# Performance work log

Hardware: AMD Instinct MI355X
Metric: run time of the kernel (lower is better)

The kernel has to match this reference:

```python
import jax, jax.numpy as jnp
import numpy as np

D_IN, D, N_HEADS, K, VOCAB = 768, 512, 8, 6, 1000
HEAD_DIM = D // N_HEADS


def setup_inputs() -> dict:
    key = jax.random.key(0)
    ks = jax.random.split(key, 16)
    B, T, L = 32, 4096, 512
    s = 0.02
    return {
        "video_features": jax.random.normal(ks[0], (B, T, D_IN), jnp.float32),
        "input_ids": jax.random.randint(ks[1], (B, L), 0, VOCAB),
        "attention_mask": jnp.ones((B, L), jnp.float32),
        # video_encoder (Linear 768->512), stored [in, out]
        "W_enc": jax.random.normal(ks[2], (D_IN, D), jnp.float32) * s,
        "b_enc": jnp.zeros((D,), jnp.float32),
        # frame_selector (Linear 512->1)
        "W_sel": jax.random.normal(ks[3], (D, 1), jnp.float32) * s,
        "b_sel": jnp.zeros((1,), jnp.float32),
        # text_encoder embedding
        "emb": jax.random.normal(ks[4], (VOCAB, D), jnp.float32) * s,
        # MultiheadAttention in/out projections
        "W_q": jax.random.normal(ks[5], (D, D), jnp.float32) * s,
        "W_k": jax.random.normal(ks[6], (D, D), jnp.float32) * s,
        "W_v": jax.random.normal(ks[7], (D, D), jnp.float32) * s,
        "b_q": jnp.zeros((D,), jnp.float32),
        "b_k": jnp.zeros((D,), jnp.float32),
        "b_v": jnp.zeros((D,), jnp.float32),
        "W_o": jax.random.normal(ks[8], (D, D), jnp.float32) * s,
        "b_o": jnp.zeros((D,), jnp.float32),
        # classifier (Linear 512->1000)
        "W_cls": jax.random.normal(ks[9], (D, VOCAB), jnp.float32) * s,
        "b_cls": jnp.zeros((VOCAB,), jnp.float32),
    }


def reference(video_features, input_ids, attention_mask, W_enc, b_enc, W_sel,
              b_sel, emb, W_q, W_k, W_v, b_q, b_k, b_v, W_o, b_o, W_cls, b_cls):
    # encode frames: [B, T, 512]
    ve = jax.nn.relu(jnp.einsum('bti,io->bto', video_features, W_enc) + b_enc)
    # frame scores [B, T] -> top-6 gather
    scores = jnp.einsum('btd,do->bto', ve, W_sel)[..., 0] + b_sel[0]
    _, top_idx = jax.lax.top_k(scores, K)                      # [B, K]
    reps = jnp.take_along_axis(ve, top_idx[:, :, None], axis=1)  # [B, K, 512]
    # text embedding (query), reps as key/value
    txt = emb[input_ids]                                       # [B, L, 512]
    B, L, _ = txt.shape
    q = (txt @ W_q + b_q).reshape(B, L, N_HEADS, HEAD_DIM)
    k = (reps @ W_k + b_k).reshape(B, K, N_HEADS, HEAD_DIM)
    v = (reps @ W_v + b_v).reshape(B, K, N_HEADS, HEAD_DIM)
    scale = 1.0 / np.sqrt(HEAD_DIM).astype(np.float32)
    attn = jax.nn.softmax(jnp.einsum('blhd,bkhd->bhlk', q, k) * scale, axis=-1)
    ctx = jnp.einsum('bhlk,bkhd->blhd', attn, v).reshape(B, L, D)
    fused = ctx @ W_o + b_o
    logits = fused @ W_cls + b_cls                             # [B, L, 1000]
    return logits, reps
```

## Files before the change

### kernel.cpp

```cpp
#include <hip/hip_runtime.h>
#include <math.h>


#define DEV __device__ __forceinline__

typedef _Float16 half8 __attribute__((ext_vector_type(8)));
typedef float f32x4v __attribute__((ext_vector_type(4)));

DEV unsigned short f2h_bits(float f) {
  union { _Float16 h; unsigned short u; } cv;
  cv.h = (_Float16)f;
  return cv.u;
}

DEV uint4 packf16x8(float4 fa, float4 fb) {
  uint4 pk;
  pk.x = (unsigned int)f2h_bits(fa.x) | ((unsigned int)f2h_bits(fa.y) << 16);
  pk.y = (unsigned int)f2h_bits(fa.z) | ((unsigned int)f2h_bits(fa.w) << 16);
  pk.z = (unsigned int)f2h_bits(fb.x) | ((unsigned int)f2h_bits(fb.y) << 16);
  pk.w = (unsigned int)f2h_bits(fb.z) | ((unsigned int)f2h_bits(fb.w) << 16);
  return pk;
}

DEV void gload16(const void* g, void* lds) {
  auto* gp = reinterpret_cast<const __attribute__((address_space(1))) unsigned int*>(
      reinterpret_cast<unsigned long long>(g));
  auto* lp = reinterpret_cast<__attribute__((address_space(3))) unsigned int*>(
      reinterpret_cast<unsigned long long>(lds));
  __builtin_amdgcn_global_load_lds(gp, lp, 16, 0, 0);
}

__global__ __launch_bounds__(256) void prep_k(
    const float* __restrict__ W_enc, unsigned short* __restrict__ WencT,
    const float* __restrict__ emb, const float* __restrict__ W_q,
    const float* __restrict__ b_q, float* __restrict__ Qe,
    const float* __restrict__ W_o, const float* __restrict__ W_cls,
    unsigned short* __restrict__ WocT, const float* __restrict__ b_o,
    const float* __restrict__ b_cls, float* __restrict__ boc) {
  __shared__ float plds[2080];
  const int blk = blockIdx.x, tid = threadIdx.x;
  if (blk < 96) {
    unsigned short* t = (unsigned short*)plds;
    const int k0 = (blk % 12) * 64, n0 = (blk / 12) * 64;
    for (int e = tid; e < 4096; e += 256) {
      int kk = e >> 6, nn = e & 63;
      t[kk * 65 + nn] = f2h_bits(W_enc[(size_t)(k0 + kk) * 512 + n0 + nn]);
    }
    __syncthreads();
    for (int e = tid; e < 4096; e += 256) {
      int nn = e >> 6, kk = e & 63;
      WencT[(size_t)(n0 + nn) * 768 + k0 + kk] = t[kk * 65 + nn];
    }
  } else if (blk < 346) {
    float* er = plds;
    const int r0 = (blk - 96) * 4;
    for (int i = tid; i < 2048; i += 256) er[i] = emb[(size_t)r0 * 512 + i];
    __syncthreads();
    const int j0 = tid, j1 = tid + 256;
    float a0[4], a1[4];
#pragma unroll
    for (int r = 0; r < 4; ++r) { a0[r] = 0.f; a1[r] = 0.f; }
    for (int i = 0; i < 512; ++i) {
      float w0 = W_q[i * 512 + j0], w1 = W_q[i * 512 + j1];
#pragma unroll
      for (int r = 0; r < 4; ++r) {
        a0[r] += er[r * 512 + i] * w0;
        a1[r] += er[r * 512 + i] * w1;
      }
    }
    float bq0 = b_q[j0], bq1 = b_q[j1];
#pragma unroll
    for (int r = 0; r < 4; ++r) {
      Qe[(size_t)(r0 + r) * 512 + j0] = a0[r] + bq0;
      Qe[(size_t)(r0 + r) * 512 + j1] = a1[r] + bq1;
    }
  } else if (blk < 474) {
    float* wr = plds;
    const int i0 = (blk - 346) * 4;
    for (int i = tid; i < 2048; i += 256) wr[i] = W_o[(size_t)i0 * 512 + i];
    __syncthreads();
    float a[4][4];
#pragma unroll
    for (int r = 0; r < 4; ++r)
#pragma unroll
      for (int c = 0; c < 4; ++c) a[r][c] = 0.f;
    for (int m = 0; m < 512; ++m) {
      float wc[4];
#pragma unroll
      for (int c = 0; c < 4; ++c) {
        int j = tid + c * 256;
        wc[c] = (j < 1000) ? W_cls[(size_t)m * 1000 + j] : 0.f;
      }
#pragma unroll
      for (int r = 0; r < 4; ++r) {
        float x = wr[r * 512 + m];
#pragma unroll
        for (int c = 0; c < 4; ++c) a[r][c] += x * wc[c];
      }
    }
#pragma unroll
    for (int r = 0; r < 4; ++r)
#pragma unroll
      for (int c = 0; c < 4; ++c) {
        int j = tid + c * 256;
        if (j < 1000) WocT[(size_t)j * 512 + i0 + r] = f2h_bits(a[r][c]);
      }
    if (blk == 346) {
      for (int i = tid; i < 24 * 512; i += 256) WocT[512000 + i] = 0;
    }
  } else {
    int j = (blk - 474) * 256 + tid;
    float s = 0.f;
    if (j < 1000) {
      for (int m = 0; m < 512; ++m) s += b_o[m] * W_cls[(size_t)m * 1000 + j];
      s += b_cls[j];
    }
    boc[j] = s;
  }
}

__global__ __launch_bounds__(512, 2) void score_gemm(
    const float* __restrict__ vf, const unsigned short* __restrict__ WencT,
    const float* __restrict__ b_enc, const float* __restrict__ W_sel,
    const float* __restrict__ b_sel, float* __restrict__ scores) {
  __shared__ unsigned short As[2][128 * 32];
  __shared__ unsigned short Bs[2][512 * 32];
  __shared__ float red[8 * 128];

  const int tid = threadIdx.x;
  const int wv = tid >> 6, lane = tid & 63;
  const int quad = lane >> 4, l15 = lane & 15;
  const int rowBase = blockIdx.x * 128;
  const int rso = ((quad ^ (l15 & 3)) << 4);
  char* const AsB0 = (char*)As[0];
  char* const AsB1 = (char*)As[1];
  char* const BsB0 = (char*)Bs[0];
  char* const BsB1 = (char*)Bs[1];

  f32x4v acc[8][4];
#pragma unroll
  for (int i = 0; i < 8; ++i)
#pragma unroll
    for (int j = 0; j < 4; ++j) acc[i][j] = (f32x4v){0.f, 0.f, 0.f, 0.f};

  const int arow = tid >> 2, aseg = tid & 3;
  const float* aSrc = vf + (size_t)(rowBase + arow) * 768 + aseg * 8;
  const int adst = arow * 64 + ((aseg ^ (arow & 3)) << 4);

  auto stage_b = [&](int kk, char* dstB) {
#pragma unroll
    for (int it = 0; it < 4; ++it) {
      int q = tid + it * 512;
      int n = q >> 2, seg = q & 3;
      gload16(WencT + (size_t)n * 768 + kk * 32 + ((seg ^ (n & 3)) << 3),
              dstB + (it * 512 + wv * 64) * 16);
    }
  };
  auto consume = [&](const char* A, const char* B) {
    half8 af[8], bf[4];
#pragma unroll
    for (int i = 0; i < 8; ++i)
      af[i] = *(const half8*)(A + (16 * i + l15) * 64 + rso);
#pragma unroll
    for (int j = 0; j < 4; ++j)
      bf[j] = *(const half8*)(B + (wv * 64 + 16 * j + l15) * 64 + rso);
#pragma unroll
    for (int i = 0; i < 8; ++i)
#pragma unroll
      for (int j = 0; j < 4; ++j)
        acc[i][j] = __builtin_amdgcn_mfma_f32_16x16x32_f16(af[i], bf[j], acc[i][j], 0, 0, 0);
  };

  stage_b(0, BsB0);
  {
    float4 fa = *(const float4*)(aSrc);
    float4 fb = *(const float4*)(aSrc + 4);
    *(uint4*)(AsB0 + adst) = packf16x8(fa, fb);
  }
  __syncthreads();
  int cur = 0;
  for (int kk = 0; kk < 23; ++kk) {
    const float* s = aSrc + (kk + 1) * 32;
    float4 fa = *(const float4*)(s);
    float4 fb = *(const float4*)(s + 4);
    char* An = cur ? AsB0 : AsB1;
    char* Bn = cur ? BsB0 : BsB1;
    stage_b(kk + 1, Bn);
    consume(cur ? AsB1 : AsB0, cur ? BsB1 : BsB0);
    *(uint4*)(An + adst) = packf16x8(fa, fb);
    __syncthreads();
    cur ^= 1;
  }
  consume(cur ? AsB1 : AsB0, cur ? BsB1 : BsB0);

  float be[4], wsv[4];
#pragma unroll
  for (int j = 0; j < 4; ++j) {
    int col = wv * 64 + 16 * j + l15;
    be[j] = b_enc[col];
    wsv[j] = W_sel[col];
  }
  float part[32];
#pragma unroll
  for (int x = 0; x < 32; ++x) part[x] = 0.f;
#pragma unroll
  for (int i = 0; i < 8; ++i)
#pragma unroll
    for (int j = 0; j < 4; ++j)
#pragma unroll
      for (int r = 0; r < 4; ++r) {
        float v = acc[i][j][r] + be[j];
        v = fmaxf(v, 0.f);
        part[i * 4 + r] += v * wsv[j];
      }
#pragma unroll
  for (int m = 1; m < 16; m <<= 1)
#pragma unroll
    for (int x = 0; x < 32; ++x) part[x] += __shfl_xor(part[x], m);
  if (l15 == 0) {
#pragma unroll
    for (int i = 0; i < 8; ++i)
#pragma unroll
      for (int r = 0; r < 4; ++r)
        red[wv * 128 + 16 * i + quad * 4 + r] = part[i * 4 + r];
  }
  __syncthreads();
  if (tid < 128) {
    float s = 0.f;
#pragma unroll
    for (int ww = 0; ww < 8; ++ww) s += red[ww * 128 + tid];
    scores[rowBase + tid] = s + b_sel[0];
  }
}

__global__ __launch_bounds__(256) void topk16(const float* __restrict__ scores,
                                              int* __restrict__ cand) {
  __shared__ float swv[4];
  __shared__ int swi[4];
  __shared__ int winner;
  const int b = blockIdx.x, tid = threadIdx.x;
  const int lane = tid & 63, w = tid >> 6;
  float v[16];
#pragma unroll
  for (int p = 0; p < 16; ++p) v[p] = scores[b * 4096 + p * 256 + tid];
  for (int r = 0; r < 16; ++r) {
    float bv = v[0];
    int bp = 0;
#pragma unroll
    for (int p = 1; p < 16; ++p)
      if (v[p] > bv) { bv = v[p]; bp = p; }
    int bi = bp * 256 + tid;
#pragma unroll
    for (int m = 1; m < 64; m <<= 1) {
      float ov = __shfl_xor(bv, m);
      int oi = __shfl_xor(bi, m);
      if (ov > bv || (ov == bv && oi < bi)) { bv = ov; bi = oi; }
    }
    if (lane == 0) { swv[w] = bv; swi[w] = bi; }
    __syncthreads();
    if (tid == 0) {
      float fv = swv[0];
      int fi = swi[0];
#pragma unroll
      for (int x = 1; x < 4; ++x)
        if (swv[x] > fv || (swv[x] == fv && swi[x] < fi)) { fv = swv[x]; fi = swi[x]; }
      cand[b * 16 + r] = fi;
      winner = fi;
    }
    __syncthreads();
    const int wi = winner;
    const int wp = wi >> 8, wt = wi & 255;
#pragma unroll
    for (int p = 0; p < 16; ++p)
      if (p == wp && tid == wt) v[p] = -3.0e38f;
    __syncthreads();
  }
}

__global__ __launch_bounds__(256) void rescore(
    const float* __restrict__ vf, const int* __restrict__ cand,
    const float* __restrict__ W_enc, const float* __restrict__ b_enc,
    const float* __restrict__ W_sel, const float* __restrict__ b_sel,
    float* __restrict__ veC, float* __restrict__ exsc) {
  __shared__ float vfs[4][768];
  __shared__ float redl[16];
  const int b = blockIdx.x, cb = blockIdx.y * 4, tid = threadIdx.x;
  for (int c = 0; c < 4; ++c) {
    int t = cand[b * 16 + cb + c];
    const float* src = vf + ((size_t)b * 4096 + t) * 768;
    for (int i = tid; i < 768; i += 256) vfs[c][i] = src[i];
  }
  __syncthreads();
  const int j0 = tid, j1 = tid + 256;
  float a0[4] = {0.f, 0.f, 0.f, 0.f}, a1[4] = {0.f, 0.f, 0.f, 0.f};
  for (int i = 0; i < 768; ++i) {
    float w0 = W_enc[(size_t)i * 512 + j0], w1 = W_enc[(size_t)i * 512 + j1];
#pragma unroll
    for (int c = 0; c < 4; ++c) {
      float x = vfs[c][i];
      a0[c] += x * w0;
      a1[c] += x * w1;
    }
  }
  float ws0 = W_sel[j0], ws1 = W_sel[j1];
  float be0 = b_enc[j0], be1 = b_enc[j1];
  float s[4];
#pragma unroll
  for (int c = 0; c < 4; ++c) {
    float v0 = fmaxf(a0[c] + be0, 0.f);
    float v1 = fmaxf(a1[c] + be1, 0.f);
    veC[((size_t)b * 16 + cb + c) * 512 + j0] = v0;
    veC[((size_t)b * 16 + cb + c) * 512 + j1] = v1;
    s[c] = v0 * ws0 + v1 * ws1;
  }
#pragma unroll
  for (int m = 1; m < 64; m <<= 1)
#pragma unroll
    for (int c = 0; c < 4; ++c) s[c] += __shfl_xor(s[c], m);
  int w = tid >> 6;
  if ((tid & 63) == 0) {
#pragma unroll
    for (int c = 0; c < 4; ++c) redl[c * 4 + w] = s[c];
  }
  __syncthreads();
  if (tid < 4)
    exsc[b * 16 + cb + tid] = redl[tid * 4 + 0] + redl[tid * 4 + 1] +
                              redl[tid * 4 + 2] + redl[tid * 4 + 3] + b_sel[0];
}

__global__ __launch_bounds__(256) void select6(
    const float* __restrict__ exsc, const int* __restrict__ cand,
    const float* __restrict__ veC, int* __restrict__ sel,
    float* __restrict__ repsOut) {
  __shared__ int selL[6];
  const int b = blockIdx.x, tid = threadIdx.x;
  if (tid == 0) {
    float v[16]; int idx[16]; bool used[16];
    for (int c = 0; c < 16; ++c) {
      v[c] = exsc[b * 16 + c];
      idx[c] = cand[b * 16 + c];
      used[c] = false;
    }
    for (int r = 0; r < 6; ++r) {
      int bi = -1;
      for (int c = 0; c < 16; ++c) {
        if (used[c]) continue;
        if (bi < 0 || v[c] > v[bi] || (v[c] == v[bi] && idx[c] < idx[bi])) bi = c;
      }
      used[bi] = true;
      selL[r] = bi;
      sel[b * 6 + r] = bi;
    }
  }
  __syncthreads();
  for (int r = 0; r < 6; ++r) {
    int c = selL[r];
    for (int i = tid; i < 512; i += 256)
      repsOut[((size_t)b * 6 + r) * 512 + i] = veC[((size_t)b * 16 + c) * 512 + i];
  }
}

__global__ __launch_bounds__(256) void kv_proj(
    const int* __restrict__ sel, const float* __restrict__ veC,
    const float* __restrict__ W_k, const float* __restrict__ W_v,
    const float* __restrict__ b_k, const float* __restrict__ b_v,
    float* __restrict__ Ks, float* __restrict__ Vs) {
  __shared__ float rep[512];
  const int br = blockIdx.x;
  const int b = br / 6;
  const int tid = threadIdx.x;
  const int c = sel[br];
  for (int i = tid; i < 512; i += 256) rep[i] = veC[((size_t)b * 16 + c) * 512 + i];
  __syncthreads();
  const int j0 = tid, j1 = tid + 256;
  float k0 = 0.f, k1 = 0.f, v0 = 0.f, v1 = 0.f;
  for (int m = 0; m < 512; ++m) {
    float x = rep[m];
    k0 += x * W_k[m * 512 + j0];
    k1 += x * W_k[m * 512 + j1];
    v0 += x * W_v[m * 512 + j0];
    v1 += x * W_v[m * 512 + j1];
  }
  Ks[(size_t)br * 512 + j0] = (k0 + b_k[j0]) * 0.125f;
  Ks[(size_t)br * 512 + j1] = (k1 + b_k[j1]) * 0.125f;
  Vs[(size_t)br * 512 + j0] = v0 + b_v[j0];
  Vs[(size_t)br * 512 + j1] = v1 + b_v[j1];
}

__global__ __launch_bounds__(256) void ctx_kernel(
    const int* __restrict__ ids, const float* __restrict__ Qe,
    const float* __restrict__ Ks, const float* __restrict__ Vs,
    unsigned short* __restrict__ CTX) {
  const int token = blockIdx.x * 4 + (threadIdx.x >> 6);
  const int lane = threadIdx.x & 63;
  const int b = token >> 9;
  const int id = ids[token];
  float q[8];
#pragma unroll
  for (int h = 0; h < 8; ++h) q[h] = Qe[(size_t)id * 512 + h * 64 + lane];
  float s[8][6];
#pragma unroll
  for (int kk = 0; kk < 6; ++kk) {
    const float* kp = Ks + ((size_t)b * 6 + kk) * 512 + lane;
    float p[8];
#pragma unroll
    for (int h = 0; h < 8; ++h) p[h] = q[h] * kp[h * 64];
#pragma unroll
    for (int m = 1; m < 64; m <<= 1)
#pragma unroll
      for (int h = 0; h < 8; ++h) p[h] += __shfl_xor(p[h], m);
#pragma unroll
    for (int h = 0; h < 8; ++h) s[h][kk] = p[h];
  }
  const float* vbase = Vs + (size_t)b * 6 * 512 + lane;
#pragma unroll
  for (int h = 0; h < 8; ++h) {
    float mx = s[h][0];
#pragma unroll
    for (int kk = 1; kk < 6; ++kk) mx = fmaxf(mx, s[h][kk]);
    float e[6], sum = 0.f;
#pragma unroll
    for (int kk = 0; kk < 6; ++kk) { e[kk] = __expf(s[h][kk] - mx); sum += e[kk]; }
    float c = 0.f;
#pragma unroll
    for (int kk = 0; kk < 6; ++kk) c += e[kk] * vbase[(size_t)kk * 512 + h * 64];
    c *= (1.f / sum);
    CTX[(size_t)token * 512 + h * 64 + lane] = f2h_bits(c);
  }
}

__global__ __launch_bounds__(512, 2) void logits_gemm(
    const unsigned short* __restrict__ CTX, const unsigned short* __restrict__ WocT,
    const float* __restrict__ boc, float* __restrict__ out) {
  __shared__ unsigned short As[2][128 * 32];
  __shared__ unsigned short Bs[2][512 * 32];
  const int tid = threadIdx.x;
  const int wv = tid >> 6, lane = tid & 63;
  const int quad = lane >> 4, l15 = lane & 15;
  const int rowBase = blockIdx.x * 128;
  const int n0 = blockIdx.y * 512;
  const int rso = ((quad ^ (l15 & 3)) << 4);
  char* const AsB0 = (char*)As[0];
  char* const AsB1 = (char*)As[1];
  char* const BsB0 = (char*)Bs[0];
  char* const BsB1 = (char*)Bs[1];

  f32x4v acc[8][4];
#pragma unroll
  for (int i = 0; i < 8; ++i)
#pragma unroll
    for (int j = 0; j < 4; ++j) acc[i][j] = (f32x4v){0.f, 0.f, 0.f, 0.f};

  const int arow = tid >> 2, aseg = tid & 3;

  auto stage = [&](int kk, char* An, char* Bn) {
    const int k0 = kk * 32;
    gload16(CTX + (size_t)(rowBase + arow) * 512 + k0 + ((aseg ^ (arow & 3)) << 3),
            An + (wv * 64) * 16);
#pragma unroll
    for (int it = 0; it < 4; ++it) {
      int q = tid + it * 512;
      int n = q >> 2, seg = q & 3;
      gload16(WocT + (size_t)(n0 + n) * 512 + k0 + ((seg ^ (n & 3)) << 3),
              Bn + (it * 512 + wv * 64) * 16);
    }
  };
  auto consume = [&](const char* A, const char* B) {
    half8 af[8], bf[4];
#pragma unroll
    for (int i = 0; i < 8; ++i)
      af[i] = *(const half8*)(A + (16 * i + l15) * 64 + rso);
#pragma unroll
    for (int j = 0; j < 4; ++j)
      bf[j] = *(const half8*)(B + (wv * 64 + 16 * j + l15) * 64 + rso);
#pragma unroll
    for (int i = 0; i < 8; ++i)
#pragma unroll
      for (int j = 0; j < 4; ++j)
        acc[i][j] = __builtin_amdgcn_mfma_f32_16x16x32_f16(af[i], bf[j], acc[i][j], 0, 0, 0);
  };

  stage(0, AsB0, BsB0);
  __syncthreads();
  int cur = 0;
  for (int kk = 0; kk < 15; ++kk) {
    stage(kk + 1, cur ? AsB0 : AsB1, cur ? BsB0 : BsB1);
    consume(cur ? AsB1 : AsB0, cur ? BsB1 : BsB0);
    __syncthreads();
    cur ^= 1;
  }
  consume(cur ? AsB1 : AsB0, cur ? BsB1 : BsB0);

  float bo[4];
#pragma unroll
  for (int j = 0; j < 4; ++j) bo[j] = boc[n0 + wv * 64 + 16 * j + l15];
#pragma unroll
  for (int i = 0; i < 8; ++i)
#pragma unroll
    for (int j = 0; j < 4; ++j)
#pragma unroll
      for (int r = 0; r < 4; ++r) {
        int token = rowBase + 16 * i + quad * 4 + r;
        int col = n0 + wv * 64 + 16 * j + l15;
        if (col < 1000) out[(size_t)token * 1000 + col] = acc[i][j][r] + bo[j];
      }
}

extern "C" void kernel_launch(void* const* d_in, const int* in_sizes, int n_in,
                              void* d_out, int out_size, void* d_ws, size_t ws_size,
                              hipStream_t stream) {
  (void)in_sizes; (void)n_in; (void)out_size; (void)ws_size;
  const float* vf    = (const float*)d_in[0];
  const int*   ids   = (const int*)d_in[1];
  const float* W_enc = (const float*)d_in[3];
  const float* b_enc = (const float*)d_in[4];
  const float* W_sel = (const float*)d_in[5];
  const float* b_sel = (const float*)d_in[6];
  const float* emb   = (const float*)d_in[7];
  const float* W_q   = (const float*)d_in[8];
  const float* W_k   = (const float*)d_in[9];
  const float* W_v   = (const float*)d_in[10];
  const float* b_q   = (const float*)d_in[11];
  const float* b_k   = (const float*)d_in[12];
  const float* b_v   = (const float*)d_in[13];
  const float* W_o   = (const float*)d_in[14];
  const float* b_o   = (const float*)d_in[15];
  const float* W_cls = (const float*)d_in[16];
  const float* b_cls = (const float*)d_in[17];

  float* out = (float*)d_out;
  float* reps_out = out + (size_t)16384000;

  char* p = (char*)d_ws;
  auto nxt = [&](size_t bytes) -> char* {
    char* q = p;
    p += (bytes + 255) & ~(size_t)255;
    return q;
  };
  unsigned short* WencT = (unsigned short*)nxt((size_t)512 * 768 * 2);
  unsigned short* WocT  = (unsigned short*)nxt((size_t)1024 * 512 * 2);
  unsigned short* CTX   = (unsigned short*)nxt((size_t)16384 * 512 * 2);
  float* scores = (float*)nxt((size_t)131072 * 4);
  int*   cand   = (int*)nxt((size_t)512 * 4);
  float* exsc   = (float*)nxt((size_t)512 * 4);
  float* veC    = (float*)nxt((size_t)32 * 16 * 512 * 4);
  int*   sel    = (int*)nxt((size_t)192 * 4);
  float* Ks     = (float*)nxt((size_t)98304 * 4);
  float* Vs     = (float*)nxt((size_t)98304 * 4);
  float* Qe     = (float*)nxt((size_t)512000 * 4);
  float* boc    = (float*)nxt((size_t)1024 * 4);

  hipLaunchKernelGGL(prep_k,      dim3(478),    dim3(256), 0, stream,
                     W_enc, WencT, emb, W_q, b_q, Qe, W_o, W_cls, WocT, b_o, b_cls, boc);
  hipLaunchKernelGGL(score_gemm,  dim3(1024),   dim3(512), 0, stream,
                     vf, WencT, b_enc, W_sel, b_sel, scores);
  hipLaunchKernelGGL(topk16,      dim3(32),     dim3(256), 0, stream, scores, cand);
  hipLaunchKernelGGL(rescore,     dim3(32, 4),  dim3(256), 0, stream,
                     vf, cand, W_enc, b_enc, W_sel, b_sel, veC, exsc);
  hipLaunchKernelGGL(select6,     dim3(32),     dim3(256), 0, stream, exsc, cand, veC, sel, reps_out);
  hipLaunchKernelGGL(kv_proj,     dim3(192),    dim3(256), 0, stream, sel, veC, W_k, W_v, b_k, b_v, Ks, Vs);
  hipLaunchKernelGGL(ctx_kernel,  dim3(4096),   dim3(256), 0, stream, ids, Qe, Ks, Vs, CTX);
  hipLaunchKernelGGL(logits_gemm, dim3(128, 2), dim3(512), 0, stream, CTX, WocT, boc, out);
}
```

Baseline: 979.5 us.

## Load GEMM weight fragments directly from global memory, widen K-step to 64

Both the score GEMM and the logits GEMM stop staging the weight (B) tile in LDS. Each wave now reads its B fragments straight from global memory (the weight tile is shared across blocks and should hit in cache), and only the activation tile is double-buffered in LDS with an 8-way XOR swizzle over a 64-wide K step. This cuts LDS footprint and staging traffic and halves the number of barriers. The cost is that weight loads sit on the MFMA critical path with no prefetch, so global or L2 latency may stall the math.

```diff
diff --git a/kernel.cpp b/kernel.cpp
--- a/kernel.cpp
+++ b/kernel.cpp
@@ -123,19 +123,15 @@
     const float* __restrict__ vf, const unsigned short* __restrict__ WencT,
     const float* __restrict__ b_enc, const float* __restrict__ W_sel,
     const float* __restrict__ b_sel, float* __restrict__ scores) {
-  __shared__ unsigned short As[2][128 * 32];
-  __shared__ unsigned short Bs[2][512 * 32];
+  __shared__ unsigned short As[2][128 * 64];
   __shared__ float red[8 * 128];
 
   const int tid = threadIdx.x;
   const int wv = tid >> 6, lane = tid & 63;
   const int quad = lane >> 4, l15 = lane & 15;
   const int rowBase = blockIdx.x * 128;
-  const int rso = ((quad ^ (l15 & 3)) << 4);
-  char* const AsB0 = (char*)As[0];
-  char* const AsB1 = (char*)As[1];
-  char* const BsB0 = (char*)Bs[0];
-  char* const BsB1 = (char*)Bs[1];
+  char* const A0 = (char*)As[0];
+  char* const A1 = (char*)As[1];
 
   f32x4v acc[8][4];
 #pragma unroll
@@ -144,54 +140,59 @@
     for (int j = 0; j < 4; ++j) acc[i][j] = (f32x4v){0.f, 0.f, 0.f, 0.f};
 
   const int arow = tid >> 2, aseg = tid & 3;
-  const float* aSrc = vf + (size_t)(rowBase + arow) * 768 + aseg * 8;
-  const int adst = arow * 64 + ((aseg ^ (arow & 3)) << 4);
-
-  auto stage_b = [&](int kk, char* dstB) {
-#pragma unroll
-    for (int it = 0; it < 4; ++it) {
-      int q = tid + it * 512;
-      int n = q >> 2, seg = q & 3;
-      gload16(WencT + (size_t)n * 768 + kk * 32 + ((seg ^ (n & 3)) << 3),
-              dstB + (it * 512 + wv * 64) * 16);
+  const float* aSrc = vf + (size_t)(rowBase + arow) * 768 + aseg * 16;
+  const int ad0 = arow * 128 + (((2 * aseg) ^ (arow & 7)) << 4);
+  const int ad1 = arow * 128 + (((2 * aseg + 1) ^ (arow & 7)) << 4);
+
+  auto consume = [&](const char* A, int kk) {
+#pragma unroll
+    for (int c = 0; c < 2; ++c) {
+      half8 af[8], bf[4];
+#pragma unroll
+      for (int i = 0; i < 8; ++i) {
+        int row = 16 * i + l15;
+        af[i] = *(const half8*)(A + row * 128 + ((((c << 2) | quad) ^ (row & 7)) << 4));
+      }
+#pragma unroll
+      for (int j = 0; j < 4; ++j) {
+        int n = wv * 64 + 16 * j + l15;
+        bf[j] = *(const half8*)(WencT + (size_t)n * 768 + kk * 64 + c * 32 + quad * 8);
+      }
+#pragma unroll
+      for (int i = 0; i < 8; ++i)
+#pragma unroll
+        for (int j = 0; j < 4; ++j)
+          acc[i][j] = __builtin_amdgcn_mfma_f32_16x16x32_f16(af[i], bf[j], acc[i][j], 0, 0, 0);
     }
   };
-  auto consume = [&](const char* A, const char* B) {
-    half8 af[8], bf[4];
-#pragma unroll
-    for (int i = 0; i < 8; ++i)
-      af[i] = *(const half8*)(A + (16 * i + l15) * 64 + rso);
-#pragma unroll
-    for (int j = 0; j < 4; ++j)
-      bf[j] = *(const half8*)(B + (wv * 64 + 16 * j + l15) * 64 + rso);
-#pragma unroll
-    for (int i = 0; i < 8; ++i)
-#pragma unroll
-      for (int j = 0; j < 4; ++j)
-        acc[i][j] = __builtin_amdgcn_mfma_f32_16x16x32_f16(af[i], bf[j], acc[i][j], 0, 0, 0);
-  };
-
-  stage_b(0, BsB0);
+
   {
-    float4 fa = *(const float4*)(aSrc);
-    float4 fb = *(const float4*)(aSrc + 4);
-    *(uint4*)(AsB0 + adst) = packf16x8(fa, fb);
-  }
-  __syncthreads();
-  int cur = 0;
-  for (int kk = 0; kk < 23; ++kk) {
-    const float* s = aSrc + (kk + 1) * 32;
-    float4 fa = *(const float4*)(s);
-    float4 fb = *(const float4*)(s + 4);
-    char* An = cur ? AsB0 : AsB1;
-    char* Bn = cur ? BsB0 : BsB1;
-    stage_b(kk + 1, Bn);
-    consume(cur ? AsB1 : AsB0, cur ? BsB1 : BsB0);
-    *(uint4*)(An + adst) = packf16x8(fa, fb);
-    __syncthreads();
-    cur ^= 1;
-  }
-  consume(cur ? AsB1 : AsB0, cur ? BsB1 : BsB0);
+    float4 f0 = *(const float4*)(aSrc);
+    float4 f1 = *(const float4*)(aSrc + 4);
+    float4 f2 = *(const float4*)(aSrc + 8);
+    float4 f3 = *(const float4*)(aSrc + 12);
+    *(uint4*)(A0 + ad0) = packf16x8(f0, f1);
+    *(uint4*)(A0 + ad1) = packf16x8(f2, f3);
+  }
+  __syncthreads();
+  for (int kk = 0; kk < 12; ++kk) {
+    char* const Acur = (kk & 1) ? A1 : A0;
+    char* const Anxt = (kk & 1) ? A0 : A1;
+    float4 f0, f1, f2, f3;
+    if (kk < 11) {
+      const float* s = aSrc + (kk + 1) * 64;
+      f0 = *(const float4*)(s);
+      f1 = *(const float4*)(s + 4);
+      f2 = *(const float4*)(s + 8);
+      f3 = *(const float4*)(s + 12);
+    }
+    consume(Acur, kk);
+    if (kk < 11) {
+      *(uint4*)(Anxt + ad0) = packf16x8(f0, f1);
+      *(uint4*)(Anxt + ad1) = packf16x8(f2, f3);
+    }
+    __syncthreads();
+  }
 
   float be[4], wsv[4];
 #pragma unroll
@@ -432,18 +433,14 @@
 __global__ __launch_bounds__(512, 2) void logits_gemm(
     const unsigned short* __restrict__ CTX, const unsigned short* __restrict__ WocT,
     const float* __restrict__ boc, float* __restrict__ out) {
-  __shared__ unsigned short As[2][128 * 32];
-  __shared__ unsigned short Bs[2][512 * 32];
+  __shared__ unsigned short As[2][128 * 64];
   const int tid = threadIdx.x;
   const int wv = tid >> 6, lane = tid & 63;
   const int quad = lane >> 4, l15 = lane & 15;
   const int rowBase = blockIdx.x * 128;
   const int n0 = blockIdx.y * 512;
-  const int rso = ((quad ^ (l15 & 3)) << 4);
-  char* const AsB0 = (char*)As[0];
-  char* const AsB1 = (char*)As[1];
-  char* const BsB0 = (char*)Bs[0];
-  char* const BsB1 = (char*)Bs[1];
+  char* const A0 = (char*)As[0];
+  char* const A1 = (char*)As[1];
 
   f32x4v acc[8][4];
 #pragma unroll
@@ -451,45 +448,46 @@
 #pragma unroll
     for (int j = 0; j < 4; ++j) acc[i][j] = (f32x4v){0.f, 0.f, 0.f, 0.f};
 
-  const int arow = tid >> 2, aseg = tid & 3;
-
-  auto stage = [&](int kk, char* An, char* Bn) {
-    const int k0 = kk * 32;
-    gload16(CTX + (size_t)(rowBase + arow) * 512 + k0 + ((aseg ^ (arow & 3)) << 3),
-            An + (wv * 64) * 16);
-#pragma unroll
-    for (int it = 0; it < 4; ++it) {
+  auto stage = [&](int kk, char* An) {
+#pragma unroll
+    for (int it = 0; it < 2; ++it) {
       int q = tid + it * 512;
-      int n = q >> 2, seg = q & 3;
-      gload16(WocT + (size_t)(n0 + n) * 512 + k0 + ((seg ^ (n & 3)) << 3),
-              Bn + (it * 512 + wv * 64) * 16);
+      int row = q >> 3, slot = q & 7;
+      gload16(CTX + (size_t)(rowBase + row) * 512 + kk * 64 + ((slot ^ (row & 7)) << 3),
+              An + (it * 512 + wv * 64) * 16);
     }
   };
-  auto consume = [&](const char* A, const char* B) {
-    half8 af[8], bf[4];
-#pragma unroll
-    for (int i = 0; i < 8; ++i)
-      af[i] = *(const half8*)(A + (16 * i + l15) * 64 + rso);
-#pragma unroll
-    for (int j = 0; j < 4; ++j)
-      bf[j] = *(const half8*)(B + (wv * 64 + 16 * j + l15) * 64 + rso);
-#pragma unroll
-    for (int i = 0; i < 8; ++i)
-#pragma unroll
-      for (int j = 0; j < 4; ++j)
-        acc[i][j] = __builtin_amdgcn_mfma_f32_16x16x32_f16(af[i], bf[j], acc[i][j], 0, 0, 0);
+  auto consume = [&](const char* A, int kk) {
+#pragma unroll
+    for (int c = 0; c < 2; ++c) {
+      half8 af[8], bf[4];
+#pragma unroll
+      for (int i = 0; i < 8; ++i) {
+        int row = 16 * i + l15;
+        af[i] = *(const half8*)(A + row * 128 + ((((c << 2) | quad) ^ (row & 7)) << 4));
+      }
+#pragma unroll
+      for (int j = 0; j < 4; ++j) {
+        int n = n0 + wv * 64 + 16 * j + l15;
+        bf[j] = *(const half8*)(WocT + (size_t)n * 512 + kk * 64 + c * 32 + quad * 8);
+      }
+#pragma unroll
+      for (int i = 0; i < 8; ++i)
+#pragma unroll
+        for (int j = 0; j < 4; ++j)
+          acc[i][j] = __builtin_amdgcn_mfma_f32_16x16x32_f16(af[i], bf[j], acc[i][j], 0, 0, 0);
+    }
   };
 
-  stage(0, AsB0, BsB0);
-  __syncthreads();
-  int cur = 0;
-  for (int kk = 0; kk < 15; ++kk) {
-    stage(kk + 1, cur ? AsB0 : AsB1, cur ? BsB0 : BsB1);
-    consume(cur ? AsB1 : AsB0, cur ? BsB1 : BsB0);
-    __syncthreads();
-    cur ^= 1;
-  }
-  consume(cur ? AsB1 : AsB0, cur ? BsB1 : BsB0);
+  stage(0, A0);
+  __syncthreads();
+  for (int kk = 0; kk < 8; ++kk) {
+    char* const Acur = (kk & 1) ? A1 : A0;
+    char* const Anxt = (kk & 1) ? A0 : A1;
+    if (kk < 7) stage(kk + 1, Anxt);
+    consume(Acur, kk);
+    __syncthreads();
+  }
 
   float bo[4];
 #pragma unroll
```

New measurement: 1.006 ms. +2.7%, slower.

## Split GEMM tiles across 16 waves with 2x8 wave grid

Applied to the files above, without the earlier changes.

Doubles the workgroup size of both MFMA GEMM kernels (score and logits) from 512 to 1024 threads. The 128x512 block tile is now split as a 2x8 wave grid instead of 8 waves each covering all 128 rows. This halves per-wave accumulators and A-fragment loads and spreads the fp32->fp16 A staging across more threads. The aim is more latency hiding and lower register pressure per wave. The cost is a larger workgroup and an occupancy hint of 4 blocks that LDS limits may not allow, plus more B-fragment LDS reads per block.

```diff
diff --git a/kernel.cpp b/kernel.cpp
--- a/kernel.cpp
+++ b/kernel.cpp
@@ -11,15 +11,6 @@
   union { _Float16 h; unsigned short u; } cv;
   cv.h = (_Float16)f;
   return cv.u;
-}
-
-DEV uint4 packf16x8(float4 fa, float4 fb) {
-  uint4 pk;
-  pk.x = (unsigned int)f2h_bits(fa.x) | ((unsigned int)f2h_bits(fa.y) << 16);
-  pk.y = (unsigned int)f2h_bits(fa.z) | ((unsigned int)f2h_bits(fa.w) << 16);
-  pk.z = (unsigned int)f2h_bits(fb.x) | ((unsigned int)f2h_bits(fb.y) << 16);
-  pk.w = (unsigned int)f2h_bits(fb.z) | ((unsigned int)f2h_bits(fb.w) << 16);
-  return pk;
 }
 
 DEV void gload16(const void* g, void* lds) {
@@ -119,17 +110,18 @@
   }
 }
 
-__global__ __launch_bounds__(512, 2) void score_gemm(
+__global__ __launch_bounds__(1024, 4) void score_gemm(
     const float* __restrict__ vf, const unsigned short* __restrict__ WencT,
     const float* __restrict__ b_enc, const float* __restrict__ W_sel,
     const float* __restrict__ b_sel, float* __restrict__ scores) {
   __shared__ unsigned short As[2][128 * 32];
   __shared__ unsigned short Bs[2][512 * 32];
-  __shared__ float red[8 * 128];
+  __shared__ float red[16 * 64];
 
   const int tid = threadIdx.x;
   const int wv = tid >> 6, lane = tid & 63;
   const int quad = lane >> 4, l15 = lane & 15;
+  const int wr = wv >> 3, wc = wv & 7;
   const int rowBase = blockIdx.x * 128;
   const int rso = ((quad ^ (l15 & 3)) << 4);
   char* const AsB0 = (char*)As[0];
@@ -137,57 +129,62 @@
   char* const BsB0 = (char*)Bs[0];
   char* const BsB1 = (char*)Bs[1];
 
-  f32x4v acc[8][4];
-#pragma unroll
-  for (int i = 0; i < 8; ++i)
+  f32x4v acc[4][4];
+#pragma unroll
+  for (int i = 0; i < 4; ++i)
 #pragma unroll
     for (int j = 0; j < 4; ++j) acc[i][j] = (f32x4v){0.f, 0.f, 0.f, 0.f};
 
-  const int arow = tid >> 2, aseg = tid & 3;
-  const float* aSrc = vf + (size_t)(rowBase + arow) * 768 + aseg * 8;
-  const int adst = arow * 64 + ((aseg ^ (arow & 3)) << 4);
-
+  const int arow = tid >> 3, aseg = tid & 7;
+  const float* aSrc = vf + (size_t)(rowBase + arow) * 768 + aseg * 4;
+  const int aslot = aseg >> 1, ahalf = aseg & 1;
+  const int adst = arow * 64 + ((aslot ^ (arow & 3)) << 4) + ahalf * 8;
+
+  auto packA = [&](float4 f, char* An) {
+    uint2 pk;
+    pk.x = (unsigned int)f2h_bits(f.x) | ((unsigned int)f2h_bits(f.y) << 16);
+    pk.y = (unsigned int)f2h_bits(f.z) | ((unsigned int)f2h_bits(f.w) << 16);
+    *(uint2*)(An + adst) = pk;
+  };
   auto stage_b = [&](int kk, char* dstB) {
 #pragma unroll
-    for (int it = 0; it < 4; ++it) {
-      int q = tid + it * 512;
+    for (int it = 0; it < 2; ++it) {
+      int q = tid + it * 1024;
       int n = q >> 2, seg = q & 3;
       gload16(WencT + (size_t)n * 768 + kk * 32 + ((seg ^ (n & 3)) << 3),
-              dstB + (it * 512 + wv * 64) * 16);
+              dstB + (it * 1024 + wv * 64) * 16);
     }
   };
   auto consume = [&](const char* A, const char* B) {
-    half8 af[8], bf[4];
-#pragma unroll
-    for (int i = 0; i < 8; ++i)
-      af[i] = *(const half8*)(A + (16 * i + l15) * 64 + rso);
-#pragma unroll
-    for (int j = 0; j < 4; ++j)
-      bf[j] = *(const half8*)(B + (wv * 64 + 16 * j + l15) * 64 + rso);
-#pragma unroll
-    for (int i = 0; i < 8; ++i)
+    half8 af[4], bf[4];
+#pragma unroll
+    for (int i = 0; i < 4; ++i) {
+      int row = wr * 64 + 16 * i + l15;
+      af[i] = *(const half8*)(A + row * 64 + rso);
+    }
+#pragma unroll
+    for (int j = 0; j < 4; ++j) {
+      int n = wc * 64 + 16 * j + l15;
+      bf[j] = *(const half8*)(B + n * 64 + rso);
+    }
+#pragma unroll
+    for (int i = 0; i < 4; ++i)
 #pragma unroll
       for (int j = 0; j < 4; ++j)
         acc[i][j] = __builtin_amdgcn_mfma_f32_16x16x32_f16(af[i], bf[j], acc[i][j], 0, 0, 0);
   };
 
   stage_b(0, BsB0);
-  {
-    float4 fa = *(const float4*)(aSrc);
-    float4 fb = *(const float4*)(aSrc + 4);
-    *(uint4*)(AsB0 + adst) = packf16x8(fa, fb);
-  }
+  packA(*(const float4*)(aSrc), AsB0);
   __syncthreads();
   int cur = 0;
   for (int kk = 0; kk < 23; ++kk) {
-    const float* s = aSrc + (kk + 1) * 32;
-    float4 fa = *(const float4*)(s);
-    float4 fb = *(const float4*)(s + 4);
+    float4 fa = *(const float4*)(aSrc + (kk + 1) * 32);
     char* An = cur ? AsB0 : AsB1;
     char* Bn = cur ? BsB0 : BsB1;
     stage_b(kk + 1, Bn);
     consume(cur ? AsB1 : AsB0, cur ? BsB1 : BsB0);
-    *(uint4*)(An + adst) = packf16x8(fa, fb);
+    packA(fa, An);
     __syncthreads();
     cur ^= 1;
   }
@@ -196,15 +193,15 @@
   float be[4], wsv[4];
 #pragma unroll
   for (int j = 0; j < 4; ++j) {
-    int col = wv * 64 + 16 * j + l15;
+    int col = wc * 64 + 16 * j + l15;
     be[j] = b_enc[col];
     wsv[j] = W_sel[col];
   }
-  float part[32];
-#pragma unroll
-  for (int x = 0; x < 32; ++x) part[x] = 0.f;
-#pragma unroll
-  for (int i = 0; i < 8; ++i)
+  float part[16];
+#pragma unroll
+  for (int x = 0; x < 16; ++x) part[x] = 0.f;
+#pragma unroll
+  for (int i = 0; i < 4; ++i)
 #pragma unroll
     for (int j = 0; j < 4; ++j)
 #pragma unroll
@@ -216,19 +213,20 @@
 #pragma unroll
   for (int m = 1; m < 16; m <<= 1)
 #pragma unroll
-    for (int x = 0; x < 32; ++x) part[x] += __shfl_xor(part[x], m);
+    for (int x = 0; x < 16; ++x) part[x] += __shfl_xor(part[x], m);
   if (l15 == 0) {
 #pragma unroll
-    for (int i = 0; i < 8; ++i)
+    for (int i = 0; i < 4; ++i)
 #pragma unroll
       for (int r = 0; r < 4; ++r)
-        red[wv * 128 + 16 * i + quad * 4 + r] = part[i * 4 + r];
+        red[wv * 64 + 16 * i + quad * 4 + r] = part[i * 4 + r];
   }
   __syncthreads();
   if (tid < 128) {
+    const int rh = tid >> 6, rl = tid & 63;
     float s = 0.f;
 #pragma unroll
-    for (int ww = 0; ww < 8; ++ww) s += red[ww * 128 + tid];
+    for (int ww = 0; ww < 8; ++ww) s += red[(rh * 8 + ww) * 64 + rl];
     scores[rowBase + tid] = s + b_sel[0];
   }
 }
@@ -429,7 +427,7 @@
   }
 }
 
-__global__ __launch_bounds__(512, 2) void logits_gemm(
+__global__ __launch_bounds__(1024, 4) void logits_gemm(
     const unsigned short* __restrict__ CTX, const unsigned short* __restrict__ WocT,
     const float* __restrict__ boc, float* __restrict__ out) {
   __shared__ unsigned short As[2][128 * 32];
@@ -437,6 +435,7 @@
   const int tid = threadIdx.x;
   const int wv = tid >> 6, lane = tid & 63;
   const int quad = lane >> 4, l15 = lane & 15;
+  const int wr = wv >> 3, wc = wv & 7;
   const int rowBase = blockIdx.x * 128;
   const int n0 = blockIdx.y * 512;
   const int rso = ((quad ^ (l15 & 3)) << 4);
@@ -445,9 +444,9 @@
   char* const BsB0 = (char*)Bs[0];
   char* const BsB1 = (char*)Bs[1];
 
-  f32x4v acc[8][4];
-#pragma unroll
-  for (int i = 0; i < 8; ++i)
+  f32x4v acc[4][4];
+#pragma unroll
+  for (int i = 0; i < 4; ++i)
 #pragma unroll
     for (int j = 0; j < 4; ++j) acc[i][j] = (f32x4v){0.f, 0.f, 0.f, 0.f};
 
@@ -455,26 +454,32 @@
 
   auto stage = [&](int kk, char* An, char* Bn) {
     const int k0 = kk * 32;
-    gload16(CTX + (size_t)(rowBase + arow) * 512 + k0 + ((aseg ^ (arow & 3)) << 3),
-            An + (wv * 64) * 16);
-#pragma unroll
-    for (int it = 0; it < 4; ++it) {
-      int q = tid + it * 512;
+    if (wv < 8) {
+      gload16(CTX + (size_t)(rowBase + arow) * 512 + k0 + ((aseg ^ (arow & 3)) << 3),
+              An + wv * 1024);
+    }
+#pragma unroll
+    for (int it = 0; it < 2; ++it) {
+      int q = tid + it * 1024;
       int n = q >> 2, seg = q & 3;
       gload16(WocT + (size_t)(n0 + n) * 512 + k0 + ((seg ^ (n & 3)) << 3),
-              Bn + (it * 512 + wv * 64) * 16);
+              Bn + (it * 1024 + wv * 64) * 16);
     }
   };
   auto consume = [&](const char* A, const char* B) {
-    half8 af[8], bf[4];
-#pragma unroll
-    for (int i = 0; i < 8; ++i)
-      af[i] = *(const half8*)(A + (16 * i + l15) * 64 + rso);
-#pragma unroll
-    for (int j = 0; j < 4; ++j)
-      bf[j] = *(const half8*)(B + (wv * 64 + 16 * j + l15) * 64 + rso);
-#pragma unroll
-    for (int i = 0; i < 8; ++i)
+    half8 af[4], bf[4];
+#pragma unroll
+    for (int i = 0; i < 4; ++i) {
+      int row = wr * 64 + 16 * i + l15;
+      af[i] = *(const half8*)(A + row * 64 + rso);
+    }
+#pragma unroll
+    for (int j = 0; j < 4; ++j) {
+      int n = wc * 64 + 16 * j + l15;
+      bf[j] = *(const half8*)(B + n * 64 + rso);
+    }
+#pragma unroll
+    for (int i = 0; i < 4; ++i)
 #pragma unroll
       for (int j = 0; j < 4; ++j)
         acc[i][j] = __builtin_amdgcn_mfma_f32_16x16x32_f16(af[i], bf[j], acc[i][j], 0, 0, 0);
@@ -493,15 +498,15 @@
 
   float bo[4];
 #pragma unroll
-  for (int j = 0; j < 4; ++j) bo[j] = boc[n0 + wv * 64 + 16 * j + l15];
-#pragma unroll
-  for (int i = 0; i < 8; ++i)
+  for (int j = 0; j < 4; ++j) bo[j] = boc[n0 + wc * 64 + 16 * j + l15];
+#pragma unroll
+  for (int i = 0; i < 4; ++i)
 #pragma unroll
     for (int j = 0; j < 4; ++j)
 #pragma unroll
       for (int r = 0; r < 4; ++r) {
-        int token = rowBase + 16 * i + quad * 4 + r;
-        int col = n0 + wv * 64 + 16 * j + l15;
+        int token = rowBase + wr * 64 + 16 * i + quad * 4 + r;
+        int col = n0 + wc * 64 + 16 * j + l15;
         if (col < 1000) out[(size_t)token * 1000 + col] = acc[i][j][r] + bo[j];
       }
 }
@@ -552,7 +557,7 @@
 
   hipLaunchKernelGGL(prep_k,      dim3(478),    dim3(256), 0, stream,
                      W_enc, WencT, emb, W_q, b_q, Qe, W_o, W_cls, WocT, b_o, b_cls, boc);
-  hipLaunchKernelGGL(score_gemm,  dim3(1024),   dim3(512), 0, stream,
+  hipLaunchKernelGGL(score_gemm,  dim3(1024),   dim3(1024), 0, stream,
                      vf, WencT, b_enc, W_sel, b_sel, scores);
   hipLaunchKernelGGL(topk16,      dim3(32),     dim3(256), 0, stream, scores, cand);
   hipLaunchKernelGGL(rescore,     dim3(32, 4),  dim3(256), 0, stream,
@@ -560,5 +565,5 @@
   hipLaunchKernelGGL(select6,     dim3(32),     dim3(256), 0, stream, exsc, cand, veC, sel, reps_out);
   hipLaunchKernelGGL(kv_proj,     dim3(192),    dim3(256), 0, stream, sel, veC, W_k, W_v, b_k, b_v, Ks, Vs);
   hipLaunchKernelGGL(ctx_kernel,  dim3(4096),   dim3(256), 0, stream, ids, Qe, Ks, Vs, CTX);
-  hipLaunchKernelGGL(logits_gemm, dim3(128, 2), dim3(512), 0, stream, CTX, WocT, boc, out);
-}
+  hipLaunchKernelGGL(logits_gemm, dim3(128, 2), dim3(1024), 0, stream, CTX, WocT, boc, out);
+}
```

Measured after the change: 976.6 us. No clear change (-0.3%).
